# Kernel tuning notes

Measured on AMD Instinct MI355X. Metric: run time of the kernel, lower is better.

## Reference

```python
import jax, jax.numpy as jnp
import numpy as np

DIM = 128
NUM_LAYERS = 4
VOCAB = 32000
B, S = 32, 256


def setup_inputs() -> dict:
    key = jax.random.key(0)
    ks = jax.random.split(key, 8)
    sc = 1.0 / np.sqrt(DIM)
    return {
        "x": jax.random.randint(ks[0], (B, S), 0, VOCAB, dtype=jnp.int32),
        "emb": jax.random.normal(ks[1], (VOCAB, DIM), jnp.float32) * 0.02,
        "W_ih": jax.random.uniform(ks[2], (NUM_LAYERS, 4 * DIM, DIM), jnp.float32, -sc, sc),
        "W_hh": jax.random.uniform(ks[3], (NUM_LAYERS, 4 * DIM, DIM), jnp.float32, -sc, sc),
        "b_ih": jax.random.uniform(ks[4], (NUM_LAYERS, 4 * DIM), jnp.float32, -sc, sc),
        "b_hh": jax.random.uniform(ks[5], (NUM_LAYERS, 4 * DIM), jnp.float32, -sc, sc),
        "ln_gamma": jnp.ones((DIM,), jnp.float32),
        "ln_beta": jnp.zeros((DIM,), jnp.float32),
        "head_W": jax.random.uniform(ks[6], (VOCAB, DIM), jnp.float32, -sc, sc),
        "head_b": jnp.zeros((VOCAB,), jnp.float32),
    }


def _lstm_layer(h_seq, Wih, Whh, bih, bhh):
    # h_seq: [B,S,D]. Precompute input contributions for all timesteps.
    xW = jnp.einsum("bsd,gd->bsg", h_seq, Wih) + bih + bhh  # [B,S,4D]
    xW = jnp.swapaxes(xW, 0, 1)  # [S,B,4D] for scan over time
    bsz = h_seq.shape[0]
    h0 = jnp.zeros((bsz, DIM), h_seq.dtype)
    c0 = jnp.zeros((bsz, DIM), h_seq.dtype)

    def step(carry, xw_t):
        h, c = carry
        gates = xw_t + h @ Whh.T  # [B,4D]
        i, f, g, o = jnp.split(gates, 4, axis=-1)  # torch gate order i,f,g,o
        i = jax.nn.sigmoid(i)
        f = jax.nn.sigmoid(f)
        g = jnp.tanh(g)
        o = jax.nn.sigmoid(o)
        c = f * c + i * g
        h = o * jnp.tanh(c)
        return (h, c), h

    _, hs = jax.lax.scan(step, (h0, c0), xW)
    return jnp.swapaxes(hs, 0, 1)  # [B,S,D]


def reference(x, emb, W_ih, W_hh, b_ih, b_hh, ln_gamma, ln_beta, head_W, head_b):
    h = emb[x]  # [B,S,D]
    for l in range(NUM_LAYERS):
        h = _lstm_layer(h, W_ih[l], W_hh[l], b_ih[l], b_hh[l])
    # LayerNorm over last dim (eps=1e-5, torch default)
    mu = jnp.mean(h, axis=-1, keepdims=True)
    var = jnp.mean(jnp.square(h - mu), axis=-1, keepdims=True)
    hn = (h - mu) * jax.lax.rsqrt(var + 1e-5) * ln_gamma + ln_beta
    return jnp.einsum("bsd,vd->bsv", hn, head_W) + head_b  # [B,S,V]
```

## Files before the change

### kernel.cpp

```cpp
#include <hip/hip_runtime.h>
#include <hip/hip_bf16.h>

#define DIM 128
#define G4 512
#define NL 4
#define VOCAB 32000
#define BB 32
#define SS 256
#define ROWS (BB*SS)

typedef __attribute__((ext_vector_type(8))) short short8;
typedef __attribute__((ext_vector_type(4))) float f32x4;
typedef __attribute__((ext_vector_type(4))) unsigned int uint4v;
typedef __attribute__((ext_vector_type(2))) _Float16 h2;

__device__ __forceinline__ float fexp_(float x){ return __builtin_amdgcn_exp2f(x * 1.44269504088896f); }
__device__ __forceinline__ float frcp_(float x){ return __builtin_amdgcn_rcpf(x); }
__device__ __forceinline__ float sigm_(float x){ return frcp_(1.f + fexp_(-x)); }
__device__ __forceinline__ float tanh_(float x){
    float ax = fabsf(x);
    float e = fexp_(-2.f * ax);
    float t = (1.f - e) * frcp_(1.f + e);
    return x < 0.f ? -t : t;
}
__device__ __forceinline__ h2 mkh(float a, float b){ h2 r; r.x = (_Float16)a; r.y = (_Float16)b; return r; }

#if __has_builtin(__builtin_amdgcn_fdot2)
#define FDOT2(w, d, acc) acc = __builtin_amdgcn_fdot2(w, d, acc, false);
#else
#define FDOT2(w, d, acc) acc = fmaf((float)(w).x, (float)(d).x, fmaf((float)(w).y, (float)(d).y, acc));
#endif
#define B2H(u) __builtin_bit_cast(h2, (unsigned)(u))
#define F2US(x) ((unsigned long long)__builtin_bit_cast(unsigned short, (_Float16)(x)))

#define WD32(p) h2 p##0,p##1,p##2,p##3,p##4,p##5,p##6,p##7,p##8,p##9,p##10,p##11, \
                   p##12,p##13,p##14,p##15,p##16,p##17,p##18,p##19,p##20,p##21,p##22,p##23, \
                   p##24,p##25,p##26,p##27,p##28,p##29,p##30,p##31;
#define WCVT32(p, src) { float4 t_; \
    t_=(src)[0];  p##0 =mkh(t_.x,t_.y); p##1 =mkh(t_.z,t_.w); \
    t_=(src)[1];  p##2 =mkh(t_.x,t_.y); p##3 =mkh(t_.z,t_.w); \
    t_=(src)[2];  p##4 =mkh(t_.x,t_.y); p##5 =mkh(t_.z,t_.w); \
    t_=(src)[3];  p##6 =mkh(t_.x,t_.y); p##7 =mkh(t_.z,t_.w); \
    t_=(src)[4];  p##8 =mkh(t_.x,t_.y); p##9 =mkh(t_.z,t_.w); \
    t_=(src)[5];  p##10=mkh(t_.x,t_.y); p##11=mkh(t_.z,t_.w); \
    t_=(src)[6];  p##12=mkh(t_.x,t_.y); p##13=mkh(t_.z,t_.w); \
    t_=(src)[7];  p##14=mkh(t_.x,t_.y); p##15=mkh(t_.z,t_.w); \
    t_=(src)[8];  p##16=mkh(t_.x,t_.y); p##17=mkh(t_.z,t_.w); \
    t_=(src)[9];  p##18=mkh(t_.x,t_.y); p##19=mkh(t_.z,t_.w); \
    t_=(src)[10]; p##20=mkh(t_.x,t_.y); p##21=mkh(t_.z,t_.w); \
    t_=(src)[11]; p##22=mkh(t_.x,t_.y); p##23=mkh(t_.z,t_.w); \
    t_=(src)[12]; p##24=mkh(t_.x,t_.y); p##25=mkh(t_.z,t_.w); \
    t_=(src)[13]; p##26=mkh(t_.x,t_.y); p##27=mkh(t_.z,t_.w); \
    t_=(src)[14]; p##28=mkh(t_.x,t_.y); p##29=mkh(t_.z,t_.w); \
    t_=(src)[15]; p##30=mkh(t_.x,t_.y); p##31=mkh(t_.z,t_.w); }
#define DT32(p, acc) \
    FDOT2(p##0,d0,acc)  FDOT2(p##1,d1,acc)  FDOT2(p##2,d2,acc)  FDOT2(p##3,d3,acc) \
    FDOT2(p##4,d4,acc)  FDOT2(p##5,d5,acc)  FDOT2(p##6,d6,acc)  FDOT2(p##7,d7,acc) \
    FDOT2(p##8,d8,acc)  FDOT2(p##9,d9,acc)  FDOT2(p##10,d10,acc) FDOT2(p##11,d11,acc) \
    FDOT2(p##12,d12,acc) FDOT2(p##13,d13,acc) FDOT2(p##14,d14,acc) FDOT2(p##15,d15,acc) \
    FDOT2(p##16,d16,acc) FDOT2(p##17,d17,acc) FDOT2(p##18,d18,acc) FDOT2(p##19,d19,acc) \
    FDOT2(p##20,d20,acc) FDOT2(p##21,d21,acc) FDOT2(p##22,d22,acc) FDOT2(p##23,d23,acc) \
    FDOT2(p##24,d24,acc) FDOT2(p##25,d25,acc) FDOT2(p##26,d26,acc) FDOT2(p##27,d27,acc) \
    FDOT2(p##28,d28,acc) FDOT2(p##29,d29,acc) FDOT2(p##30,d30,acc) FDOT2(p##31,d31,acc)
#define RD32(base) { const uint4v* hc_ = (const uint4v*)(base); \
    uint4v q0_=hc_[0], q1_=hc_[1], q2_=hc_[2], q3_=hc_[3], \
           q4_=hc_[4], q5_=hc_[5], q6_=hc_[6], q7_=hc_[7]; \
    d0=B2H(q0_.x); d1=B2H(q0_.y); d2=B2H(q0_.z); d3=B2H(q0_.w); \
    d4=B2H(q1_.x); d5=B2H(q1_.y); d6=B2H(q1_.z); d7=B2H(q1_.w); \
    d8=B2H(q2_.x); d9=B2H(q2_.y); d10=B2H(q2_.z); d11=B2H(q2_.w); \
    d12=B2H(q3_.x); d13=B2H(q3_.y); d14=B2H(q3_.z); d15=B2H(q3_.w); \
    d16=B2H(q4_.x); d17=B2H(q4_.y); d18=B2H(q4_.z); d19=B2H(q4_.w); \
    d20=B2H(q5_.x); d21=B2H(q5_.y); d22=B2H(q5_.z); d23=B2H(q5_.w); \
    d24=B2H(q6_.x); d25=B2H(q6_.y); d26=B2H(q6_.z); d27=B2H(q6_.w); \
    d28=B2H(q7_.x); d29=B2H(q7_.y); d30=B2H(q7_.z); d31=B2H(q7_.w); }

#define W_DECL_ALL \
    float4 w0,w1,w2,w3,w4,w5,w6,w7,w8,w9,w10,w11,w12,w13,w14,w15, \
           w16,w17,w18,w19,w20,w21,w22,w23,w24,w25,w26,w27,w28,w29,w30,w31;
#define W_LOAD(i) w##i = wr[i];
#define W_LOAD_ALL \
    W_LOAD(0) W_LOAD(1) W_LOAD(2) W_LOAD(3) W_LOAD(4) W_LOAD(5) W_LOAD(6) W_LOAD(7) \
    W_LOAD(8) W_LOAD(9) W_LOAD(10) W_LOAD(11) W_LOAD(12) W_LOAD(13) W_LOAD(14) W_LOAD(15) \
    W_LOAD(16) W_LOAD(17) W_LOAD(18) W_LOAD(19) W_LOAD(20) W_LOAD(21) W_LOAD(22) W_LOAD(23) \
    W_LOAD(24) W_LOAD(25) W_LOAD(26) W_LOAD(27) W_LOAD(28) W_LOAD(29) W_LOAD(30) W_LOAD(31)
#define FMA1(i, acc) acc = fmaf(h4[i].x, w##i.x, fmaf(h4[i].y, w##i.y, \
                      fmaf(h4[i].z, w##i.z, fmaf(h4[i].w, w##i.w, acc))));
#define DOT128(a0,a1,a2,a3) \
    FMA1(0,a0) FMA1(1,a0) FMA1(2,a0) FMA1(3,a0) FMA1(4,a0) FMA1(5,a0) FMA1(6,a0) FMA1(7,a0) \
    FMA1(8,a1) FMA1(9,a1) FMA1(10,a1) FMA1(11,a1) FMA1(12,a1) FMA1(13,a1) FMA1(14,a1) FMA1(15,a1) \
    FMA1(16,a2) FMA1(17,a2) FMA1(18,a2) FMA1(19,a2) FMA1(20,a2) FMA1(21,a2) FMA1(22,a2) FMA1(23,a2) \
    FMA1(24,a3) FMA1(25,a3) FMA1(26,a3) FMA1(27,a3) FMA1(28,a3) FMA1(29,a3) FMA1(30,a3) FMA1(31,a3)

__global__ void k_zero(int* __restrict__ f){ if (threadIdx.x < 96) f[threadIdx.x] = 0; }

__global__ void k_embed(const int* __restrict__ x, const float* __restrict__ emb,
                        float* __restrict__ hseq){
    int i = blockIdx.x * blockDim.x + threadIdx.x;
    int row = i >> 5;
    int d4  = i & 31;
    int tok = x[row];
    ((float4*)hseq)[i] = ((const float4*)emb)[tok * 32 + d4];
}

__global__ __launch_bounds__(512, 2) void k_xw(const float* __restrict__ hseq,
                                               const float* Wih,
                                               const float* __restrict__ bih,
                                               const float* __restrict__ bhh,
                                               float* xw){
    __shared__ float hs[32 * DIM];
    int g = threadIdx.x;
    int r0 = blockIdx.x * 32;
    {
        const float4* src = (const float4*)(hseq + (size_t)r0 * DIM);
        float4* dst = (float4*)hs;
        for (int j = g; j < 32 * 32; j += 512) dst[j] = src[j];
    }
    int gg = ((g & 3) << 7) + (g >> 2);
    const float4* wr = (const float4*)(Wih + (size_t)gg * DIM);
    W_DECL_ALL
    W_LOAD_ALL
    float bias = bih[gg] + bhh[gg];
    __syncthreads();
    for (int r = 0; r < 32; ++r){
        const float4* h4 = (const float4*)(hs + r * DIM);
        float a0 = bias, a1 = 0.f, a2 = 0.f, a3 = 0.f;
        DOT128(a0, a1, a2, a3)
        xw[(size_t)(r0 + r) * G4 + g] = (a0 + a1) + (a2 + a3);
    }
}

#define SCAN_STEP(XC, CH, I) { \
        h2 d0,d1,d2,d3,d4,d5,d6,d7,d8,d9,d10,d11,d12,d13,d14,d15, \
           d16,d17,d18,d19,d20,d21,d22,d23,d24,d25,d26,d27,d28,d29,d30,d31; \
        float s0 = XC.x, s1 = XC.y; \
        RD32(&hb[p][0]) \
        DT32(pA, s0) DT32(pC, s1) \
        RD32(&hb[p][64]) \
        DT32(pB, s0) DT32(pD, s1) \
        float o0 = __shfl_xor(s0, 1), o1 = __shfl_xor(s1, 1); \
        float i_pre = w ? o0 : s0, f_pre = w ? o1 : s1; \
        float g_pre = w ? s0 : o0, o_pre = w ? s1 : o1; \
        float iv = sigm_(i_pre), fv = sigm_(f_pre); \
        float gv = tanh_(g_pre), ov = sigm_(o_pre); \
        cc = fv * cc + iv * gv; \
        float h = ov * tanh_(cc); \
        if (!w) hb[p ^ 1][ci] = (_Float16)h; \
        else    stg[(CH) & 1][I][ci] = h; \
        __syncthreads(); \
        p ^= 1; }

#define XN_DOT(I) { \
        h2 d0,d1,d2,d3,d4,d5,d6,d7,d8,d9,d10,d11,d12,d13,d14,d15, \
           d16,d17,d18,d19,d20,d21,d22,d23,d24,d25,d26,d27,d28,d29,d30,d31; \
        float nx = biasv.x, ny = biasv.y; \
        RD32(hpF + (I) * 128) \
        DT32(pE, nx) DT32(pG, ny) \
        RD32(hpF + (I) * 128 + 64) \
        DT32(pF, nx) DT32(pH, ny) \
        xn##I.x = nx; xn##I.y = ny; }

__global__ __launch_bounds__(256, 1) void k_fused(
    const float* __restrict__ xw0,
    const float* Wih, const float* Whh,
    const float* __restrict__ bih, const float* __restrict__ bhh,
    unsigned long long* hf16,
    float* hseq3,
    int* flags)
{
    __shared__ _Float16 hb[2][DIM];
    __shared__ float    stg[2][16][DIM];
    __shared__ __align__(16) unsigned long long hp[512];
    const int tid = threadIdx.x;
    const int l = blockIdx.x >> 5, b = blockIdx.x & 31;
    const int ci = tid >> 1, w = tid & 1;
    const _Float16* hpF = (const _Float16*)hp;

    WD32(pA) WD32(pB) WD32(pC) WD32(pD)
    {
        const float* Wl = Whh + (size_t)l * G4 * DIM;
        const float4* r0 = (const float4*)(Wl + (size_t)((2 * w    ) * DIM + ci) * DIM);
        const float4* r1 = (const float4*)(Wl + (size_t)((2 * w + 1) * DIM + ci) * DIM);
        WCVT32(pA, r0) WCVT32(pB, r0 + 16)
        WCVT32(pC, r1) WCVT32(pD, r1 + 16)
    }
    WD32(pE) WD32(pF) WD32(pG) WD32(pH)
    float2 biasv = {0.f, 0.f};
    if (l > 0){
        const float* Vl = Wih + (size_t)l * G4 * DIM;
        const float4* q0 = (const float4*)(Vl + (size_t)((2 * w    ) * DIM + ci) * DIM);
        const float4* q1 = (const float4*)(Vl + (size_t)((2 * w + 1) * DIM + ci) * DIM);
        WCVT32(pE, q0) WCVT32(pF, q0 + 16)
        WCVT32(pG, q1) WCVT32(pH, q1 + 16)
        biasv.x = bih[l * G4 + (2 * w    ) * DIM + ci] + bhh[l * G4 + (2 * w    ) * DIM + ci];
        biasv.y = bih[l * G4 + (2 * w + 1) * DIM + ci] + bhh[l * G4 + (2 * w + 1) * DIM + ci];
    }
    unsigned long long*       pub = hf16 + (size_t)(l * 32 + b) * 8192;
    const unsigned long long* src = hf16 + (size_t)((l - 1) * 32 + b) * 8192;
    int* myflag = flags + (l * 32 + b);
    const int* inflag = flags + ((l - 1) * 32 + b);
    const float2* xw2 = (const float2*)(xw0 + (size_t)b * SS * G4);
    float* hout = hseq3 + (size_t)b * SS * DIM;

    float cc = 0.f;
    if (tid < DIM) hb[0][tid] = (_Float16)0.f;
    __syncthreads();
    int p = 0;
    int seen = 0;
    float2 xq0,xq1,xq2,xq3,xq4,xq5,xq6,xq7,xq8,xq9,xq10,xq11,xq12,xq13,xq14,xq15;
    float2 xn0,xn1,xn2,xn3,xn4,xn5,xn6,xn7,xn8,xn9,xn10,xn11,xn12,xn13,xn14,xn15;

#define BLOCK_WAIT(TGT) { int t_ = (TGT); if (seen < t_){ \
        if (tid == 0){ while (__hip_atomic_load(inflag, __ATOMIC_ACQUIRE, \
            __HIP_MEMORY_SCOPE_AGENT) < t_) __builtin_amdgcn_s_sleep(4); } \
        __syncthreads(); seen = t_; } }
#define STAGE(C) { const unsigned long long* s_ = src + (size_t)(C) * 512; \
        hp[tid]       = __hip_atomic_load(s_ + tid,       __ATOMIC_RELAXED, __HIP_MEMORY_SCOPE_AGENT); \
        hp[tid + 256] = __hip_atomic_load(s_ + tid + 256, __ATOMIC_RELAXED, __HIP_MEMORY_SCOPE_AGENT); }
#define FLUSH_PUB(C) { \
    _Pragma("unroll") \
    for (int j = 0; j < 2; ++j){ \
        int idx = j * 256 + tid; \
        int r = idx >> 5, c4 = idx & 31; \
        float4 v = *(const float4*)&stg[(C) & 1][r][c4 * 4]; \
        unsigned long long bits = F2US(v.x) | (F2US(v.y) << 16) | (F2US(v.z) << 32) | (F2US(v.w) << 48); \
        __hip_atomic_store(pub + (size_t)((C) * 16 + r) * 32 + c4, bits, \
                           __ATOMIC_RELAXED, __HIP_MEMORY_SCOPE_AGENT); \
    } }
#define FLUSH_F32(C) { \
    _Pragma("unroll") \
    for (int j = 0; j < 2; ++j){ \
        int idx = j * 256 + tid; \
        int r = idx >> 5, c4 = idx & 31; \
        float4 v = *(const float4*)&stg[(C) & 1][r][c4 * 4]; \
        *(float4*)(hout + (size_t)((C) * 16 + r) * DIM + c4 * 4) = v; \
    } }
#define XQ_FROM_XN \
    xq0=xn0; xq1=xn1; xq2=xn2; xq3=xn3; xq4=xn4; xq5=xn5; xq6=xn6; xq7=xn7; \
    xq8=xn8; xq9=xn9; xq10=xn10; xq11=xn11; xq12=xn12; xq13=xn13; xq14=xn14; xq15=xn15;

    if (l > 0){
        BLOCK_WAIT(1)
        STAGE(0)
        __syncthreads();
        XN_DOT(0)  XN_DOT(1)  XN_DOT(2)  XN_DOT(3)  XN_DOT(4)  XN_DOT(5)  XN_DOT(6)  XN_DOT(7)
        XN_DOT(8)  XN_DOT(9)  XN_DOT(10) XN_DOT(11) XN_DOT(12) XN_DOT(13) XN_DOT(14) XN_DOT(15)
        XQ_FROM_XN
    }

#pragma unroll 1
    for (int c = 0; c < 16; ++c){
        if (c > 0){
            if (l < 3) FLUSH_PUB(c - 1)
            else       FLUSH_F32(c - 1)
        }
        if (l == 0){
            const int t0 = c * 16;
            xq0  = xw2[(t0 +  0) * 256 + tid]; xq1  = xw2[(t0 +  1) * 256 + tid];
            xq2  = xw2[(t0 +  2) * 256 + tid]; xq3  = xw2[(t0 +  3) * 256 + tid];
            xq4  = xw2[(t0 +  4) * 256 + tid]; xq5  = xw2[(t0 +  5) * 256 + tid];
            xq6  = xw2[(t0 +  6) * 256 + tid]; xq7  = xw2[(t0 +  7) * 256 + tid];
            xq8  = xw2[(t0 +  8) * 256 + tid]; xq9  = xw2[(t0 +  9) * 256 + tid];
            xq10 = xw2[(t0 + 10) * 256 + tid]; xq11 = xw2[(t0 + 11) * 256 + tid];
            xq12 = xw2[(t0 + 12) * 256 + tid]; xq13 = xw2[(t0 + 13) * 256 + tid];
            xq14 = xw2[(t0 + 14) * 256 + tid]; xq15 = xw2[(t0 + 15) * 256 + tid];
        } else if (c < 15){
            BLOCK_WAIT(c + 2)
            STAGE(c + 1)
        }
        __syncthreads();
        if (l < 3 && c > 0 && tid == 0)
            __hip_atomic_store(myflag, c, __ATOMIC_RELEASE, __HIP_MEMORY_SCOPE_AGENT);
        const bool doXN = (l > 0) && (c < 15);
        if (doXN) XN_DOT(0)   SCAN_STEP(xq0,  c, 0)
        if (doXN) XN_DOT(1)   SCAN_STEP(xq1,  c, 1)
        if (doXN) XN_DOT(2)   SCAN_STEP(xq2,  c, 2)
        if (doXN) XN_DOT(3)   SCAN_STEP(xq3,  c, 3)
        if (doXN) XN_DOT(4)   SCAN_STEP(xq4,  c, 4)
        if (doXN) XN_DOT(5)   SCAN_STEP(xq5,  c, 5)
        if (doXN) XN_DOT(6)   SCAN_STEP(xq6,  c, 6)
        if (doXN) XN_DOT(7)   SCAN_STEP(xq7,  c, 7)
        if (doXN) XN_DOT(8)   SCAN_STEP(xq8,  c, 8)
        if (doXN) XN_DOT(9)   SCAN_STEP(xq9,  c, 9)
        if (doXN) XN_DOT(10)  SCAN_STEP(xq10, c, 10)
        if (doXN) XN_DOT(11)  SCAN_STEP(xq11, c, 11)
        if (doXN) XN_DOT(12)  SCAN_STEP(xq12, c, 12)
        if (doXN) XN_DOT(13)  SCAN_STEP(xq13, c, 13)
        if (doXN) XN_DOT(14)  SCAN_STEP(xq14, c, 14)
        if (doXN) XN_DOT(15)  SCAN_STEP(xq15, c, 15)
        if (doXN){ XQ_FROM_XN }
    }
    if (l < 3){
        FLUSH_PUB(15)
        __syncthreads();
        if (tid == 0)
            __hip_atomic_store(myflag, 16, __ATOMIC_RELEASE, __HIP_MEMORY_SCOPE_AGENT);
    } else {
        FLUSH_F32(15)
    }
#undef BLOCK_WAIT
#undef STAGE
#undef FLUSH_PUB
#undef FLUSH_F32
#undef XQ_FROM_XN
}

__global__ void k_ln(const float* __restrict__ hseq, const float* __restrict__ gamma,
                     const float* __restrict__ beta, __hip_bfloat16* __restrict__ hn){
    int wid = threadIdx.x >> 6;
    int lane = threadIdx.x & 63;
    int row = blockIdx.x * 4 + wid;
    float2 hv = ((const float2*)(hseq + (size_t)row * DIM))[lane];
    float s = hv.x + hv.y;
    float sq = fmaf(hv.x, hv.x, hv.y * hv.y);
    for (int off = 32; off; off >>= 1){ s += __shfl_xor(s, off); sq += __shfl_xor(sq, off); }
    float mu = s * (1.f / 128.f);
    float var = sq * (1.f / 128.f) - mu * mu;
    float inv = rsqrtf(var + 1e-5f);
    float2 gv = ((const float2*)gamma)[lane];
    float2 bv = ((const float2*)beta)[lane];
    __hip_bfloat162 pr;
    pr.x = __float2bfloat16((hv.x - mu) * inv * gv.x + bv.x);
    pr.y = __float2bfloat16((hv.y - mu) * inv * gv.y + bv.y);
    ((__hip_bfloat162*)hn)[(size_t)row * 64 + lane] = pr;
}

__global__ void k_cvt(const float* __restrict__ w, __hip_bfloat16* __restrict__ wb){
    int i = blockIdx.x * blockDim.x + threadIdx.x;
    float4 v = ((const float4*)w)[i];
    __hip_bfloat162 p0, p1;
    p0.x = __float2bfloat16(v.x); p0.y = __float2bfloat16(v.y);
    p1.x = __float2bfloat16(v.z); p1.y = __float2bfloat16(v.w);
    ((__hip_bfloat162*)wb)[2 * i]     = p0;
    ((__hip_bfloat162*)wb)[2 * i + 1] = p1;
}

__global__ __launch_bounds__(256) void k_head(const __hip_bfloat16* __restrict__ hn,
                                              const __hip_bfloat16* __restrict__ wb,
                                              const float* __restrict__ head_b,
                                              float* __restrict__ out){
    int bn = blockIdx.x;
    int bm = blockIdx.y;
    int wid = threadIdx.x >> 6;
    int lane = threadIdx.x & 63;
    int wr = wid >> 1, wc = wid & 1;
    int row0 = bm * 128 + wr * 64;
    int col0 = bn * 128 + wc * 64;
    const short* A  = (const short*)hn;
    const short* Bp = (const short*)wb;
    f32x4 zero = {0.f, 0.f, 0.f, 0.f};
    f32x4 acc[4][4];
#pragma unroll
    for (int i = 0; i < 4; ++i)
#pragma unroll
        for (int j = 0; j < 4; ++j) acc[i][j] = zero;
    int lrow = lane & 15;
    int kgr = (lane >> 4) * 8;
#pragma unroll
    for (int ks = 0; ks < 4; ++ks){
        short8 a[4], bf[4];
#pragma unroll
        for (int mi = 0; mi < 4; ++mi)
            a[mi] = *(const short8*)(A + (size_t)(row0 + mi * 16 + lrow) * DIM + ks * 32 + kgr);
#pragma unroll
        for (int ni = 0; ni < 4; ++ni)
            bf[ni] = *(const short8*)(Bp + (size_t)(col0 + ni * 16 + lrow) * DIM + ks * 32 + kgr);
#pragma unroll
        for (int mi = 0; mi < 4; ++mi)
#pragma unroll
            for (int ni = 0; ni < 4; ++ni)
                acc[mi][ni] = __builtin_amdgcn_mfma_f32_16x16x32_bf16(bf[ni], a[mi], acc[mi][ni], 0, 0, 0);
    }
    int csub = (lane >> 4) * 4;
#pragma unroll
    for (int ni = 0; ni < 4; ++ni){
        int cbase = col0 + ni * 16 + csub;
        float4 b4 = ((const float4*)head_b)[cbase >> 2];
#pragma unroll
        for (int mi = 0; mi < 4; ++mi){
            int row = row0 + mi * 16 + lrow;
            f32x4 v;
            v[0] = acc[mi][ni][0] + b4.x;
            v[1] = acc[mi][ni][1] + b4.y;
            v[2] = acc[mi][ni][2] + b4.z;
            v[3] = acc[mi][ni][3] + b4.w;
            __builtin_nontemporal_store(v, (f32x4*)(out + (size_t)row * VOCAB + cbase));
        }
    }
}

extern "C" void kernel_launch(void* const* d_in, const int* in_sizes, int n_in,
                              void* d_out, int out_size, void* d_ws, size_t ws_size,
                              hipStream_t stream){
    const int*   x     = (const int*)  d_in[0];
    const float* emb   = (const float*)d_in[1];
    const float* Wih   = (const float*)d_in[2];
    const float* Whh   = (const float*)d_in[3];
    const float* bih   = (const float*)d_in[4];
    const float* bhh   = (const float*)d_in[5];
    const float* gamma = (const float*)d_in[6];
    const float* beta  = (const float*)d_in[7];
    const float* headW = (const float*)d_in[8];
    const float* headb = (const float*)d_in[9];
    float* out = (float*)d_out;

    char* ws = (char*)d_ws;
    float* xw0  = (float*)ws;
    float* hseq = (float*)(ws + (16u << 20));
    __hip_bfloat16* hn = (__hip_bfloat16*)(ws + (20u << 20));
    __hip_bfloat16* wb = (__hip_bfloat16*)(ws + (22u << 20));

    char* ob = (char*)d_out;
    unsigned long long* hf16 = (unsigned long long*)ob;
    int* flags = (int*)(ob + (6u << 20));

    k_embed<<<1024, 256, 0, stream>>>(x, emb, hseq);
    k_cvt  <<<4000, 256, 0, stream>>>(headW, wb);
    k_xw   <<<256, 512, 0, stream>>>(hseq, Wih, bih, bhh, xw0);
    k_zero <<<1, 128, 0, stream>>>(flags);
    k_fused<<<128, 256, 0, stream>>>(xw0, Wih, Whh, bih, bhh, hf16, hseq, flags);
    k_ln   <<<2048, 256, 0, stream>>>(hseq, gamma, beta, hn);
    k_head <<<dim3(250, 64), 256, 0, stream>>>(hn, wb, headb, out);
}
```

Measured before the change: 782.8 us.

## Fuse LayerNorm and vocab head GEMM into persistent LSTM kernel with flag pipelining

Layer-3 LSTM blocks now apply LayerNorm inline and write bf16 normalized rows, signalling per-chunk completion through global counters. 128 extra blocks in the same launch run the head GEMM chunk by chunk as time-step slices become ready. This overlaps the 1 GB logits write with the recurrent scan and drops the separate LN and head launches. The layer-0 input projection is also stored in fp16 to halve its traffic, at some precision cost. The extra blocks spin-wait on flags, so the scheme depends on all 256 blocks being co-resident.

Measured after the change: 984.9 us. +25.8%, slower.

```diff
diff --git a/kernel.cpp b/kernel.cpp
--- a/kernel.cpp
+++ b/kernel.cpp
@@ -24,6 +24,15 @@
     return x < 0.f ? -t : t;
 }
 __device__ __forceinline__ h2 mkh(float a, float b){ h2 r; r.x = (_Float16)a; r.y = (_Float16)b; return r; }
+__device__ __forceinline__ unsigned long long f2bf_(float f){
+    unsigned u = __float_as_uint(f);
+    u += 0x7fffu + ((u >> 16) & 1u);
+    return (unsigned long long)(u >> 16);
+}
+__device__ __forceinline__ float2 c2f(unsigned u){
+    h2 v = __builtin_bit_cast(h2, u);
+    float2 r; r.x = (float)v.x; r.y = (float)v.y; return r;
+}
 
 #if __has_builtin(__builtin_amdgcn_fdot2)
 #define FDOT2(w, d, acc) acc = __builtin_amdgcn_fdot2(w, d, acc, false);
@@ -91,7 +100,7 @@
     FMA1(16,a2) FMA1(17,a2) FMA1(18,a2) FMA1(19,a2) FMA1(20,a2) FMA1(21,a2) FMA1(22,a2) FMA1(23,a2) \
     FMA1(24,a3) FMA1(25,a3) FMA1(26,a3) FMA1(27,a3) FMA1(28,a3) FMA1(29,a3) FMA1(30,a3) FMA1(31,a3)
 
-__global__ void k_zero(int* __restrict__ f){ if (threadIdx.x < 96) f[threadIdx.x] = 0; }
+__global__ void k_zero(int* __restrict__ f){ if (threadIdx.x < 112) f[threadIdx.x] = 0; }
 
 __global__ void k_embed(const int* __restrict__ x, const float* __restrict__ emb,
                         float* __restrict__ hseq){
@@ -106,7 +115,7 @@
                                                const float* Wih,
                                                const float* __restrict__ bih,
                                                const float* __restrict__ bhh,
-                                               float* xw){
+                                               unsigned short* xwh){
     __shared__ float hs[32 * DIM];
     int g = threadIdx.x;
     int r0 = blockIdx.x * 32;
@@ -125,7 +134,8 @@
         const float4* h4 = (const float4*)(hs + r * DIM);
         float a0 = bias, a1 = 0.f, a2 = 0.f, a3 = 0.f;
         DOT128(a0, a1, a2, a3)
-        xw[(size_t)(r0 + r) * G4 + g] = (a0 + a1) + (a2 + a3);
+        float v = (a0 + a1) + (a2 + a3);
+        xwh[(size_t)(r0 + r) * G4 + g] = __builtin_bit_cast(unsigned short, (_Float16)v);
     }
 }
 
@@ -160,54 +170,59 @@
         xn##I.x = nx; xn##I.y = ny; }
 
 __global__ __launch_bounds__(256, 1) void k_fused(
-    const float* __restrict__ xw0,
+    const unsigned short* __restrict__ xw0h,
     const float* Wih, const float* Whh,
     const float* __restrict__ bih, const float* __restrict__ bhh,
     unsigned long long* hf16,
-    float* hseq3,
-    int* flags)
+    int* flags,
+    const float* __restrict__ gamma, const float* __restrict__ beta,
+    __hip_bfloat16* hnb,
+    const __hip_bfloat16* __restrict__ wbp, const float* __restrict__ head_b,
+    float* __restrict__ out, int* gflag)
 {
     __shared__ _Float16 hb[2][DIM];
     __shared__ float    stg[2][16][DIM];
     __shared__ __align__(16) unsigned long long hp[512];
     const int tid = threadIdx.x;
-    const int l = blockIdx.x >> 5, b = blockIdx.x & 31;
-    const int ci = tid >> 1, w = tid & 1;
-    const _Float16* hpF = (const _Float16*)hp;
-
-    WD32(pA) WD32(pB) WD32(pC) WD32(pD)
-    {
-        const float* Wl = Whh + (size_t)l * G4 * DIM;
-        const float4* r0 = (const float4*)(Wl + (size_t)((2 * w    ) * DIM + ci) * DIM);
-        const float4* r1 = (const float4*)(Wl + (size_t)((2 * w + 1) * DIM + ci) * DIM);
-        WCVT32(pA, r0) WCVT32(pB, r0 + 16)
-        WCVT32(pC, r1) WCVT32(pD, r1 + 16)
-    }
-    WD32(pE) WD32(pF) WD32(pG) WD32(pH)
-    float2 biasv = {0.f, 0.f};
-    if (l > 0){
-        const float* Vl = Wih + (size_t)l * G4 * DIM;
-        const float4* q0 = (const float4*)(Vl + (size_t)((2 * w    ) * DIM + ci) * DIM);
-        const float4* q1 = (const float4*)(Vl + (size_t)((2 * w + 1) * DIM + ci) * DIM);
-        WCVT32(pE, q0) WCVT32(pF, q0 + 16)
-        WCVT32(pG, q1) WCVT32(pH, q1 + 16)
-        biasv.x = bih[l * G4 + (2 * w    ) * DIM + ci] + bhh[l * G4 + (2 * w    ) * DIM + ci];
-        biasv.y = bih[l * G4 + (2 * w + 1) * DIM + ci] + bhh[l * G4 + (2 * w + 1) * DIM + ci];
-    }
-    unsigned long long*       pub = hf16 + (size_t)(l * 32 + b) * 8192;
-    const unsigned long long* src = hf16 + (size_t)((l - 1) * 32 + b) * 8192;
-    int* myflag = flags + (l * 32 + b);
-    const int* inflag = flags + ((l - 1) * 32 + b);
-    const float2* xw2 = (const float2*)(xw0 + (size_t)b * SS * G4);
-    float* hout = hseq3 + (size_t)b * SS * DIM;
-
-    float cc = 0.f;
-    if (tid < DIM) hb[0][tid] = (_Float16)0.f;
-    __syncthreads();
-    int p = 0;
-    int seen = 0;
-    float2 xq0,xq1,xq2,xq3,xq4,xq5,xq6,xq7,xq8,xq9,xq10,xq11,xq12,xq13,xq14,xq15;
-    float2 xn0,xn1,xn2,xn3,xn4,xn5,xn6,xn7,xn8,xn9,xn10,xn11,xn12,xn13,xn14,xn15;
+
+    if (blockIdx.x < 128){
+        const int l = blockIdx.x >> 5, b = blockIdx.x & 31;
+        const int ci = tid >> 1, w = tid & 1;
+        const _Float16* hpF = (const _Float16*)hp;
+
+        WD32(pA) WD32(pB) WD32(pC) WD32(pD)
+        {
+            const float* Wl = Whh + (size_t)l * G4 * DIM;
+            const float4* r0 = (const float4*)(Wl + (size_t)((2 * w    ) * DIM + ci) * DIM);
+            const float4* r1 = (const float4*)(Wl + (size_t)((2 * w + 1) * DIM + ci) * DIM);
+            WCVT32(pA, r0) WCVT32(pB, r0 + 16)
+            WCVT32(pC, r1) WCVT32(pD, r1 + 16)
+        }
+        WD32(pE) WD32(pF) WD32(pG) WD32(pH)
+        float2 biasv = {0.f, 0.f};
+        if (l > 0){
+            const float* Vl = Wih + (size_t)l * G4 * DIM;
+            const float4* q0 = (const float4*)(Vl + (size_t)((2 * w    ) * DIM + ci) * DIM);
+            const float4* q1 = (const float4*)(Vl + (size_t)((2 * w + 1) * DIM + ci) * DIM);
+            WCVT32(pE, q0) WCVT32(pF, q0 + 16)
+            WCVT32(pG, q1) WCVT32(pH, q1 + 16)
+            biasv.x = bih[l * G4 + (2 * w    ) * DIM + ci] + bhh[l * G4 + (2 * w    ) * DIM + ci];
+            biasv.y = bih[l * G4 + (2 * w + 1) * DIM + ci] + bhh[l * G4 + (2 * w + 1) * DIM + ci];
+        }
+        unsigned long long*       pub = hf16 + (size_t)(l * 32 + b) * 8192;
+        const unsigned long long* src = hf16 + (size_t)((l - 1) * 32 + b) * 8192;
+        int* myflag = flags + (l * 32 + b);
+        const int* inflag = flags + ((l - 1) * 32 + b);
+        const unsigned* xwu = (const unsigned*)xw0h + (size_t)b * SS * 256;
+        unsigned long long* hn8 = (unsigned long long*)hnb;
+
+        float cc = 0.f;
+        if (tid < DIM) hb[0][tid] = (_Float16)0.f;
+        __syncthreads();
+        int p = 0;
+        int seen = 0;
+        float2 xq0,xq1,xq2,xq3,xq4,xq5,xq6,xq7,xq8,xq9,xq10,xq11,xq12,xq13,xq14,xq15;
+        float2 xn0,xn1,xn2,xn3,xn4,xn5,xn6,xn7,xn8,xn9,xn10,xn11,xn12,xn13,xn14,xn15;
 
 #define BLOCK_WAIT(TGT) { int t_ = (TGT); if (seen < t_){ \
         if (tid == 0){ while (__hip_atomic_load(inflag, __ATOMIC_ACQUIRE, \
@@ -226,102 +241,176 @@
         __hip_atomic_store(pub + (size_t)((C) * 16 + r) * 32 + c4, bits, \
                            __ATOMIC_RELAXED, __HIP_MEMORY_SCOPE_AGENT); \
     } }
-#define FLUSH_F32(C) { \
+#define FLUSH_LN(C) { \
     _Pragma("unroll") \
     for (int j = 0; j < 2; ++j){ \
         int idx = j * 256 + tid; \
         int r = idx >> 5, c4 = idx & 31; \
         float4 v = *(const float4*)&stg[(C) & 1][r][c4 * 4]; \
-        *(float4*)(hout + (size_t)((C) * 16 + r) * DIM + c4 * 4) = v; \
+        float s_ = (v.x + v.y) + (v.z + v.w); \
+        float q_ = fmaf(v.x, v.x, fmaf(v.y, v.y, fmaf(v.z, v.z, v.w * v.w))); \
+        s_ += __shfl_xor(s_, 1);  q_ += __shfl_xor(q_, 1); \
+        s_ += __shfl_xor(s_, 2);  q_ += __shfl_xor(q_, 2); \
+        s_ += __shfl_xor(s_, 4);  q_ += __shfl_xor(q_, 4); \
+        s_ += __shfl_xor(s_, 8);  q_ += __shfl_xor(q_, 8); \
+        s_ += __shfl_xor(s_, 16); q_ += __shfl_xor(q_, 16); \
+        float mu_ = s_ * (1.f / 128.f); \
+        float var_ = q_ * (1.f / 128.f) - mu_ * mu_; \
+        float inv_ = rsqrtf(var_ + 1e-5f); \
+        float4 gv_ = ((const float4*)gamma)[c4]; \
+        float4 bv_ = ((const float4*)beta)[c4]; \
+        unsigned long long bits = \
+              f2bf_((v.x - mu_) * inv_ * gv_.x + bv_.x) \
+            | (f2bf_((v.y - mu_) * inv_ * gv_.y + bv_.y) << 16) \
+            | (f2bf_((v.z - mu_) * inv_ * gv_.z + bv_.z) << 32) \
+            | (f2bf_((v.w - mu_) * inv_ * gv_.w + bv_.w) << 48); \
+        int grow = b * 256 + (C) * 16 + r; \
+        __hip_atomic_store(hn8 + (size_t)grow * 32 + c4, bits, \
+                           __ATOMIC_RELAXED, __HIP_MEMORY_SCOPE_AGENT); \
     } }
 #define XQ_FROM_XN \
     xq0=xn0; xq1=xn1; xq2=xn2; xq3=xn3; xq4=xn4; xq5=xn5; xq6=xn6; xq7=xn7; \
     xq8=xn8; xq9=xn9; xq10=xn10; xq11=xn11; xq12=xn12; xq13=xn13; xq14=xn14; xq15=xn15;
 
-    if (l > 0){
-        BLOCK_WAIT(1)
-        STAGE(0)
-        __syncthreads();
-        XN_DOT(0)  XN_DOT(1)  XN_DOT(2)  XN_DOT(3)  XN_DOT(4)  XN_DOT(5)  XN_DOT(6)  XN_DOT(7)
-        XN_DOT(8)  XN_DOT(9)  XN_DOT(10) XN_DOT(11) XN_DOT(12) XN_DOT(13) XN_DOT(14) XN_DOT(15)
-        XQ_FROM_XN
-    }
+        if (l > 0){
+            BLOCK_WAIT(1)
+            STAGE(0)
+            __syncthreads();
+            XN_DOT(0)  XN_DOT(1)  XN_DOT(2)  XN_DOT(3)  XN_DOT(4)  XN_DOT(5)  XN_DOT(6)  XN_DOT(7)
+            XN_DOT(8)  XN_DOT(9)  XN_DOT(10) XN_DOT(11) XN_DOT(12) XN_DOT(13) XN_DOT(14) XN_DOT(15)
+            XQ_FROM_XN
+        }
 
 #pragma unroll 1
-    for (int c = 0; c < 16; ++c){
-        if (c > 0){
-            if (l < 3) FLUSH_PUB(c - 1)
-            else       FLUSH_F32(c - 1)
-        }
-        if (l == 0){
-            const int t0 = c * 16;
-            xq0  = xw2[(t0 +  0) * 256 + tid]; xq1  = xw2[(t0 +  1) * 256 + tid];
-            xq2  = xw2[(t0 +  2) * 256 + tid]; xq3  = xw2[(t0 +  3) * 256 + tid];
-            xq4  = xw2[(t0 +  4) * 256 + tid]; xq5  = xw2[(t0 +  5) * 256 + tid];
-            xq6  = xw2[(t0 +  6) * 256 + tid]; xq7  = xw2[(t0 +  7) * 256 + tid];
-            xq8  = xw2[(t0 +  8) * 256 + tid]; xq9  = xw2[(t0 +  9) * 256 + tid];
-            xq10 = xw2[(t0 + 10) * 256 + tid]; xq11 = xw2[(t0 + 11) * 256 + tid];
-            xq12 = xw2[(t0 + 12) * 256 + tid]; xq13 = xw2[(t0 + 13) * 256 + tid];
-            xq14 = xw2[(t0 + 14) * 256 + tid]; xq15 = xw2[(t0 + 15) * 256 + tid];
-        } else if (c < 15){
-            BLOCK_WAIT(c + 2)
-            STAGE(c + 1)
-        }
-        __syncthreads();
-        if (l < 3 && c > 0 && tid == 0)
-            __hip_atomic_store(myflag, c, __ATOMIC_RELEASE, __HIP_MEMORY_SCOPE_AGENT);
-        const bool doXN = (l > 0) && (c < 15);
-        if (doXN) XN_DOT(0)   SCAN_STEP(xq0,  c, 0)
-        if (doXN) XN_DOT(1)   SCAN_STEP(xq1,  c, 1)
-        if (doXN) XN_DOT(2)   SCAN_STEP(xq2,  c, 2)
-        if (doXN) XN_DOT(3)   SCAN_STEP(xq3,  c, 3)
-        if (doXN) XN_DOT(4)   SCAN_STEP(xq4,  c, 4)
-        if (doXN) XN_DOT(5)   SCAN_STEP(xq5,  c, 5)
-        if (doXN) XN_DOT(6)   SCAN_STEP(xq6,  c, 6)
-        if (doXN) XN_DOT(7)   SCAN_STEP(xq7,  c, 7)
-        if (doXN) XN_DOT(8)   SCAN_STEP(xq8,  c, 8)
-        if (doXN) XN_DOT(9)   SCAN_STEP(xq9,  c, 9)
-        if (doXN) XN_DOT(10)  SCAN_STEP(xq10, c, 10)
-        if (doXN) XN_DOT(11)  SCAN_STEP(xq11, c, 11)
-        if (doXN) XN_DOT(12)  SCAN_STEP(xq12, c, 12)
-        if (doXN) XN_DOT(13)  SCAN_STEP(xq13, c, 13)
-        if (doXN) XN_DOT(14)  SCAN_STEP(xq14, c, 14)
-        if (doXN) XN_DOT(15)  SCAN_STEP(xq15, c, 15)
-        if (doXN){ XQ_FROM_XN }
-    }
-    if (l < 3){
-        FLUSH_PUB(15)
-        __syncthreads();
-        if (tid == 0)
-            __hip_atomic_store(myflag, 16, __ATOMIC_RELEASE, __HIP_MEMORY_SCOPE_AGENT);
-    } else {
-        FLUSH_F32(15)
-    }
+        for (int c = 0; c < 16; ++c){
+            if (c > 0){
+                if (l < 3) FLUSH_PUB(c - 1)
+                else       FLUSH_LN(c - 1)
+            }
+            if (l == 0){
+                const int t0 = c * 16;
+                unsigned u0  = xwu[(t0 +  0) * 256 + tid], u1  = xwu[(t0 +  1) * 256 + tid],
+                         u2  = xwu[(t0 +  2) * 256 + tid], u3  = xwu[(t0 +  3) * 256 + tid],
+                         u4  = xwu[(t0 +  4) * 256 + tid], u5  = xwu[(t0 +  5) * 256 + tid],
+                         u6  = xwu[(t0 +  6) * 256 + tid], u7  = xwu[(t0 +  7) * 256 + tid],
+                         u8  = xwu[(t0 +  8) * 256 + tid], u9  = xwu[(t0 +  9) * 256 + tid],
+                         u10 = xwu[(t0 + 10) * 256 + tid], u11 = xwu[(t0 + 11) * 256 + tid],
+                         u12 = xwu[(t0 + 12) * 256 + tid], u13 = xwu[(t0 + 13) * 256 + tid],
+                         u14 = xwu[(t0 + 14) * 256 + tid], u15 = xwu[(t0 + 15) * 256 + tid];
+                xq0  = c2f(u0);  xq1  = c2f(u1);  xq2  = c2f(u2);  xq3  = c2f(u3);
+                xq4  = c2f(u4);  xq5  = c2f(u5);  xq6  = c2f(u6);  xq7  = c2f(u7);
+                xq8  = c2f(u8);  xq9  = c2f(u9);  xq10 = c2f(u10); xq11 = c2f(u11);
+                xq12 = c2f(u12); xq13 = c2f(u13); xq14 = c2f(u14); xq15 = c2f(u15);
+            } else if (c < 15){
+                BLOCK_WAIT(c + 2)
+                STAGE(c + 1)
+            }
+            __syncthreads();
+            if (c > 0 && tid == 0){
+                if (l < 3) __hip_atomic_store(myflag, c, __ATOMIC_RELEASE, __HIP_MEMORY_SCOPE_AGENT);
+                else       __hip_atomic_fetch_add(&gflag[c - 1], 1, __ATOMIC_RELEASE, __HIP_MEMORY_SCOPE_AGENT);
+            }
+            const bool doXN = (l > 0) && (c < 15);
+            if (doXN) XN_DOT(0)   SCAN_STEP(xq0,  c, 0)
+            if (doXN) XN_DOT(1)   SCAN_STEP(xq1,  c, 1)
+            if (doXN) XN_DOT(2)   SCAN_STEP(xq2,  c, 2)
+            if (doXN) XN_DOT(3)   SCAN_STEP(xq3,  c, 3)
+            if (doXN) XN_DOT(4)   SCAN_STEP(xq4,  c, 4)
+            if (doXN) XN_DOT(5)   SCAN_STEP(xq5,  c, 5)
+            if (doXN) XN_DOT(6)   SCAN_STEP(xq6,  c, 6)
+            if (doXN) XN_DOT(7)   SCAN_STEP(xq7,  c, 7)
+            if (doXN) XN_DOT(8)   SCAN_STEP(xq8,  c, 8)
+            if (doXN) XN_DOT(9)   SCAN_STEP(xq9,  c, 9)
+            if (doXN) XN_DOT(10)  SCAN_STEP(xq10, c, 10)
+            if (doXN) XN_DOT(11)  SCAN_STEP(xq11, c, 11)
+            if (doXN) XN_DOT(12)  SCAN_STEP(xq12, c, 12)
+            if (doXN) XN_DOT(13)  SCAN_STEP(xq13, c, 13)
+            if (doXN) XN_DOT(14)  SCAN_STEP(xq14, c, 14)
+            if (doXN) XN_DOT(15)  SCAN_STEP(xq15, c, 15)
+            if (doXN){ XQ_FROM_XN }
+        }
+        if (l < 3){
+            FLUSH_PUB(15)
+            __syncthreads();
+            if (tid == 0)
+                __hip_atomic_store(myflag, 16, __ATOMIC_RELEASE, __HIP_MEMORY_SCOPE_AGENT);
+        } else {
+            FLUSH_LN(15)
+            __syncthreads();
+            if (tid == 0)
+                __hip_atomic_fetch_add(&gflag[15], 1, __ATOMIC_RELEASE, __HIP_MEMORY_SCOPE_AGENT);
+        }
 #undef BLOCK_WAIT
 #undef STAGE
 #undef FLUSH_PUB
-#undef FLUSH_F32
+#undef FLUSH_LN
 #undef XQ_FROM_XN
-}
-
-__global__ void k_ln(const float* __restrict__ hseq, const float* __restrict__ gamma,
-                     const float* __restrict__ beta, __hip_bfloat16* __restrict__ hn){
-    int wid = threadIdx.x >> 6;
-    int lane = threadIdx.x & 63;
-    int row = blockIdx.x * 4 + wid;
-    float2 hv = ((const float2*)(hseq + (size_t)row * DIM))[lane];
-    float s = hv.x + hv.y;
-    float sq = fmaf(hv.x, hv.x, hv.y * hv.y);
-    for (int off = 32; off; off >>= 1){ s += __shfl_xor(s, off); sq += __shfl_xor(sq, off); }
-    float mu = s * (1.f / 128.f);
-    float var = sq * (1.f / 128.f) - mu * mu;
-    float inv = rsqrtf(var + 1e-5f);
-    float2 gv = ((const float2*)gamma)[lane];
-    float2 bv = ((const float2*)beta)[lane];
-    __hip_bfloat162 pr;
-    pr.x = __float2bfloat16((hv.x - mu) * inv * gv.x + bv.x);
-    pr.y = __float2bfloat16((hv.y - mu) * inv * gv.y + bv.y);
-    ((__hip_bfloat162*)hn)[(size_t)row * 64 + lane] = pr;
+    } else {
+        (void)__hip_atomic_load(&gflag[0], __ATOMIC_ACQUIRE, __HIP_MEMORY_SCOPE_AGENT);
+        const int widx = blockIdx.x - 128;
+        const int wid = tid >> 6, lane = tid & 63;
+        const int wr = wid >> 1, wc = wid & 1;
+        const int lrow = lane & 15, kgr = (lane >> 4) * 8;
+        const int csub = (lane >> 4) * 4;
+        const short* A  = (const short*)hnb;
+        const short* Bp = (const short*)wbp;
+        int doneNeed = 0;
+        for (int idx = widx; idx < 16000; idx += 128){
+            const int t0 = idx / 2000;
+            const int rr = idx % 2000;
+            const int bn = rr >> 3, g = rr & 7;
+            const int need = 2 * (t0 + 1);
+            if (need > doneNeed){
+                if (tid == 0){
+                    while (__hip_atomic_load(&gflag[need - 1], __ATOMIC_ACQUIRE,
+                                             __HIP_MEMORY_SCOPE_AGENT) < 32)
+                        __builtin_amdgcn_s_sleep(8);
+                }
+                __syncthreads();
+                doneNeed = need;
+            }
+            const int col0 = bn * 128 + wc * 64;
+            const int rbase = (g * 4 + wr * 2) * 256 + t0 * 32;
+            f32x4 zero = {0.f, 0.f, 0.f, 0.f};
+            f32x4 acc[4][4];
+#pragma unroll
+            for (int i = 0; i < 4; ++i)
+#pragma unroll
+                for (int j = 0; j < 4; ++j) acc[i][j] = zero;
+#pragma unroll
+            for (int ks = 0; ks < 4; ++ks){
+                short8 a[4], bf[4];
+#pragma unroll
+                for (int mi = 0; mi < 4; ++mi){
+                    int grow = rbase + (mi >> 1) * 256 + (mi & 1) * 16 + lrow;
+                    a[mi] = *(const short8*)(A + (size_t)grow * DIM + ks * 32 + kgr);
+                }
+#pragma unroll
+                for (int ni = 0; ni < 4; ++ni)
+                    bf[ni] = *(const short8*)(Bp + (size_t)(col0 + ni * 16 + lrow) * DIM + ks * 32 + kgr);
+#pragma unroll
+                for (int mi = 0; mi < 4; ++mi)
+#pragma unroll
+                    for (int ni = 0; ni < 4; ++ni)
+                        acc[mi][ni] = __builtin_amdgcn_mfma_f32_16x16x32_bf16(bf[ni], a[mi], acc[mi][ni], 0, 0, 0);
+            }
+#pragma unroll
+            for (int ni = 0; ni < 4; ++ni){
+                int cbase = col0 + ni * 16 + csub;
+                float4 b4 = ((const float4*)head_b)[cbase >> 2];
+#pragma unroll
+                for (int mi = 0; mi < 4; ++mi){
+                    int grow = rbase + (mi >> 1) * 256 + (mi & 1) * 16 + lrow;
+                    f32x4 v;
+                    v[0] = acc[mi][ni][0] + b4.x;
+                    v[1] = acc[mi][ni][1] + b4.y;
+                    v[2] = acc[mi][ni][2] + b4.z;
+                    v[3] = acc[mi][ni][3] + b4.w;
+                    __builtin_nontemporal_store(v, (f32x4*)(out + (size_t)grow * VOCAB + cbase));
+                }
+            }
+        }
+    }
 }
 
 __global__ void k_cvt(const float* __restrict__ w, __hip_bfloat16* __restrict__ wb){
@@ -332,60 +421,6 @@
     p1.x = __float2bfloat16(v.z); p1.y = __float2bfloat16(v.w);
     ((__hip_bfloat162*)wb)[2 * i]     = p0;
     ((__hip_bfloat162*)wb)[2 * i + 1] = p1;
-}
-
-__global__ __launch_bounds__(256) void k_head(const __hip_bfloat16* __restrict__ hn,
-                                              const __hip_bfloat16* __restrict__ wb,
-                                              const float* __restrict__ head_b,
-                                              float* __restrict__ out){
-    int bn = blockIdx.x;
-    int bm = blockIdx.y;
-    int wid = threadIdx.x >> 6;
-    int lane = threadIdx.x & 63;
-    int wr = wid >> 1, wc = wid & 1;
-    int row0 = bm * 128 + wr * 64;
-    int col0 = bn * 128 + wc * 64;
-    const short* A  = (const short*)hn;
-    const short* Bp = (const short*)wb;
-    f32x4 zero = {0.f, 0.f, 0.f, 0.f};
-    f32x4 acc[4][4];
-#pragma unroll
-    for (int i = 0; i < 4; ++i)
-#pragma unroll
-        for (int j = 0; j < 4; ++j) acc[i][j] = zero;
-    int lrow = lane & 15;
-    int kgr = (lane >> 4) * 8;
-#pragma unroll
-    for (int ks = 0; ks < 4; ++ks){
-        short8 a[4], bf[4];
-#pragma unroll
-        for (int mi = 0; mi < 4; ++mi)
-            a[mi] = *(const short8*)(A + (size_t)(row0 + mi * 16 + lrow) * DIM + ks * 32 + kgr);
-#pragma unroll
-        for (int ni = 0; ni < 4; ++ni)
-            bf[ni] = *(const short8*)(Bp + (size_t)(col0 + ni * 16 + lrow) * DIM + ks * 32 + kgr);
-#pragma unroll
-        for (int mi = 0; mi < 4; ++mi)
-#pragma unroll
-            for (int ni = 0; ni < 4; ++ni)
-                acc[mi][ni] = __builtin_amdgcn_mfma_f32_16x16x32_bf16(bf[ni], a[mi], acc[mi][ni], 0, 0, 0);
-    }
-    int csub = (lane >> 4) * 4;
-#pragma unroll
-    for (int ni = 0; ni < 4; ++ni){
-        int cbase = col0 + ni * 16 + csub;
-        float4 b4 = ((const float4*)head_b)[cbase >> 2];
-#pragma unroll
-        for (int mi = 0; mi < 4; ++mi){
-            int row = row0 + mi * 16 + lrow;
-            f32x4 v;
-            v[0] = acc[mi][ni][0] + b4.x;
-            v[1] = acc[mi][ni][1] + b4.y;
-            v[2] = acc[mi][ni][2] + b4.z;
-            v[3] = acc[mi][ni][3] + b4.w;
-            __builtin_nontemporal_store(v, (f32x4*)(out + (size_t)row * VOCAB + cbase));
-        }
-    }
 }
 
 extern "C" void kernel_launch(void* const* d_in, const int* in_sizes, int n_in,
@@ -404,20 +439,18 @@
     float* out = (float*)d_out;
 
     char* ws = (char*)d_ws;
-    float* xw0  = (float*)ws;
-    float* hseq = (float*)(ws + (16u << 20));
-    __hip_bfloat16* hn = (__hip_bfloat16*)(ws + (20u << 20));
-    __hip_bfloat16* wb = (__hip_bfloat16*)(ws + (22u << 20));
-
-    char* ob = (char*)d_out;
-    unsigned long long* hf16 = (unsigned long long*)ob;
-    int* flags = (int*)(ob + (6u << 20));
+    unsigned short* xw0h = (unsigned short*)ws;
+    float* hseq = (float*)(ws + (8u << 20));
+    unsigned long long* hf16 = (unsigned long long*)(ws + (12u << 20));
+    __hip_bfloat16* hn = (__hip_bfloat16*)(ws + (18u << 20));
+    __hip_bfloat16* wb = (__hip_bfloat16*)(ws + (20u << 20));
+    int* flags = (int*)(ws + (28u << 20));
+    int* gflag = flags + 96;
 
     k_embed<<<1024, 256, 0, stream>>>(x, emb, hseq);
     k_cvt  <<<4000, 256, 0, stream>>>(headW, wb);
-    k_xw   <<<256, 512, 0, stream>>>(hseq, Wih, bih, bhh, xw0);
+    k_xw   <<<256, 512, 0, stream>>>(hseq, Wih, bih, bhh, xw0h);
     k_zero <<<1, 128, 0, stream>>>(flags);
-    k_fused<<<128, 256, 0, stream>>>(xw0, Wih, Whh, bih, bhh, hf16, hseq, flags);
-    k_ln   <<<2048, 256, 0, stream>>>(hseq, gamma, beta, hn);
-    k_head <<<dim3(250, 64), 256, 0, stream>>>(hn, wb, headb, out);
-}
+    k_fused<<<256, 256, 0, stream>>>(xw0h, Wih, Whh, bih, bhh, hf16, flags,
+                                     gamma, beta, hn, wb, headb, out, gflag);
+}
```
